# Optimization experiments

Measured on AMD Instinct MI355X. Metric: run time of the kernel, lower is better.

The kernel has to match this reference:

```python
import jax, jax.numpy as jnp
import numpy as np

N_FEAT = 256
NUM_HEADS = 8
EPS = 1e-12  # torch F.normalize default eps


def setup_inputs() -> dict:
    key = jax.random.key(0)
    k1, k2, k3 = jax.random.split(key, 3)
    b, c, h, w = 1, N_FEAT, 64, 64
    x = jax.random.normal(k1, (b, c, h, w), dtype=jnp.float32)
    # 1x1 convs == channel GEMMs; store as (out_ch, in_ch) matrices
    w_qkv = jax.random.normal(k2, (3 * c, c), dtype=jnp.float32) * (1.0 / np.sqrt(c))
    w_proj = jax.random.normal(k3, (c, c), dtype=jnp.float32) * (1.0 / np.sqrt(c))
    temperature = jnp.ones((NUM_HEADS, 1, 1), dtype=jnp.float32)
    return {"x": x, "w_qkv": w_qkv, "w_proj": w_proj, "temperature": temperature}


def _l2norm(t):
    n = jnp.linalg.norm(t, axis=-1, keepdims=True)
    return t / jnp.maximum(n, EPS)


def reference(x, w_qkv, w_proj, temperature):
    b, c, h, w = x.shape
    heads = temperature.shape[0]
    d = c // heads
    hw = h * w
    xf = x.reshape(b, c, hw)
    # qkv 1x1 conv: (b, 3c, hw)
    qkv = jnp.einsum('oc,bcs->bos', w_qkv, xf)
    qkv = qkv.reshape(b, 3, heads, d, hw)
    q, k, v = qkv[:, 0], qkv[:, 1], qkv[:, 2]  # (b, heads, d, hw)
    q = jnp.swapaxes(q, -2, -1)  # (b, heads, hw, d)
    k = jnp.swapaxes(k, -2, -1)
    v = jnp.swapaxes(v, -2, -1)
    q = _l2norm(q)
    k = _l2norm(k)
    attn = jnp.einsum('bhsd,bhtd->bhst', q, k) * temperature[None]  # (b, heads, hw, hw)
    attn = jax.nn.softmax(attn, axis=-1)
    out = jnp.einsum('bhst,bhtd->bhsd', attn, v)  # (b, heads, hw, d)
    # faithful to torch: permute(0,2,1,3).reshape(b,c,h,w)
    out = out.transpose(0, 2, 1, 3).reshape(b, c, h, w)
    out = jnp.einsum('oc,bchw->bohw', w_proj, out)
    return out
```

## Files before the change

kernel.cpp:

```cpp
#include <hip/hip_runtime.h>
#include <stdint.h>

#define HW 4096
#define NH 8
#define NSPLIT 4
#define TSPLIT (HW / NSPLIT)

typedef __attribute__((ext_vector_type(8))) short short8;
typedef __attribute__((ext_vector_type(4))) short s4b;
typedef __attribute__((ext_vector_type(4))) float floatx4;

__device__ inline float bf2f(uint16_t u) {
  union { uint32_t i; float f; } v; v.i = ((uint32_t)u) << 16; return v.f;
}
__device__ inline uint16_t f2bf(float f) {
  union { float f; uint32_t i; } v; v.f = f;
  uint32_t u = v.i; u += 0x7fffu + ((u >> 16) & 1u); return (uint16_t)(u >> 16);
}
__device__ inline uint32_t pk2(float a, float b) {
  return (uint32_t)f2bf(a) | ((uint32_t)f2bf(b) << 16);
}
__device__ inline uint32_t asu(float f) { union { float f; uint32_t i; } v; v.f = f; return v.i; }
__device__ inline uint32_t pk2r(float a, float b) {
#if __has_builtin(__builtin_amdgcn_cvt_pk_bf16_f32)
  union { short2 s; uint32_t u; } x;
  x.s = __builtin_amdgcn_cvt_pk_bf16_f32(a, b);
  return x.u;
#else
  return __builtin_amdgcn_perm(asu(b) + 0x8000u, asu(a) + 0x8000u, 0x07060302u);
#endif
}
__device__ inline s4b mk_s4(uint32_t lo, uint32_t hi) {
  union { uint32_t u[2]; s4b s; } x; x.u[0] = lo; x.u[1] = hi; return x.s;
}
__device__ inline floatx4 mfma16(s4b a, s4b b, floatx4 c) {
#if __has_builtin(__builtin_amdgcn_mfma_f32_16x16x16bf16_1k)
  return __builtin_amdgcn_mfma_f32_16x16x16bf16_1k(a, b, c, 0, 0, 0);
#else
  floatx4 d = c;
  asm volatile("v_mfma_f32_16x16x16_bf16 %0, %1, %2, %0" : "+v"(d) : "v"(a), "v"(b));
  return d;
#endif
}
__device__ inline bool is_f32(const uint32_t* Tp32) { return (Tp32[0] & 0xFFFFu) == 0u; }
__device__ inline float read_temp(const void* Tp, int h) {
  if (is_f32((const uint32_t*)Tp)) return ((const float*)Tp)[h];
  return bf2f(((const uint16_t*)Tp)[h]);
}

__global__ __launch_bounds__(256) void k_transpose(const void* __restrict__ X,
                                                   uint16_t* __restrict__ Xt,
                                                   const uint32_t* __restrict__ Tp32) {
  __shared__ uint16_t tile[64 * 66];
  int t = threadIdx.x;
  int s0 = blockIdx.x * 64, c0 = blockIdx.y * 64;
  {
    int cl = t >> 2, sc = (t & 3) * 16;
    uint32_t* l32 = (uint32_t*)tile;
    int base = (cl * 66 + sc) >> 1;
    if (is_f32(Tp32)) {
      const float4* x4 = (const float4*)((const float*)X + (c0 + cl) * HW + s0 + sc);
      float4 a = x4[0], b = x4[1], c = x4[2], d = x4[3];
      l32[base + 0] = pk2(a.x, a.y); l32[base + 1] = pk2(a.z, a.w);
      l32[base + 2] = pk2(b.x, b.y); l32[base + 3] = pk2(b.z, b.w);
      l32[base + 4] = pk2(c.x, c.y); l32[base + 5] = pk2(c.z, c.w);
      l32[base + 6] = pk2(d.x, d.y); l32[base + 7] = pk2(d.z, d.w);
    } else {
      const uint4* xp = (const uint4*)((const uint16_t*)X + (c0 + cl) * HW + s0 + sc);
      uint4 a = xp[0], b = xp[1];
      l32[base + 0] = a.x; l32[base + 1] = a.y; l32[base + 2] = a.z; l32[base + 3] = a.w;
      l32[base + 4] = b.x; l32[base + 5] = b.y; l32[base + 6] = b.z; l32[base + 7] = b.w;
    }
  }
  __syncthreads();
  {
    int sl = t >> 2, cc = (t & 3) * 16;
    uint32_t wbuf[8];
#pragma unroll
    for (int j = 0; j < 8; ++j) {
      uint32_t lo = tile[(cc + 2 * j) * 66 + sl];
      uint32_t hi = tile[(cc + 2 * j + 1) * 66 + sl];
      wbuf[j] = lo | (hi << 16);
    }
    uint4* op = (uint4*)(Xt + (s0 + sl) * 256 + c0 + cc);
    op[0] = make_uint4(wbuf[0], wbuf[1], wbuf[2], wbuf[3]);
    op[1] = make_uint4(wbuf[4], wbuf[5], wbuf[6], wbuf[7]);
  }
}

__global__ __launch_bounds__(256) void k_gemm_qkv(const void* __restrict__ A,
                                                  const uint16_t* __restrict__ Bt,
                                                  const void* __restrict__ Tp,
                                                  uint16_t* __restrict__ Qr,
                                                  uint16_t* __restrict__ Kr,
                                                  uint16_t* __restrict__ Vr) {
  __shared__ uint16_t sA[128 * 64];
  __shared__ uint16_t sB[64 * 64];
  int tid = threadIdx.x;
  int w = tid >> 6, lane = tid & 63, lm = lane & 15, qd = lane >> 4;
  int n0 = blockIdx.x * 64, m0 = blockIdx.y * 128;
  bool aF32 = is_f32((const uint32_t*)Tp);
  floatx4 acc[2][4];
#pragma unroll
  for (int i = 0; i < 2; ++i)
#pragma unroll
    for (int j = 0; j < 4; ++j) acc[i][j] = (floatx4){0.f, 0.f, 0.f, 0.f};

  for (int k0 = 0; k0 < 256; k0 += 64) {
    __syncthreads();
#pragma unroll
    for (int r = 0; r < 4; ++r) {
      int ch = r * 256 + tid; int row = ch >> 3, c8 = ch & 7;
      uint4 v;
      if (aF32) {
        const float4* s4 = (const float4*)((const float*)A + (m0 + row) * 256 + k0 + c8 * 8);
        float4 a = s4[0], b = s4[1];
        v = make_uint4(pk2(a.x, a.y), pk2(a.z, a.w), pk2(b.x, b.y), pk2(b.z, b.w));
      } else {
        v = *(const uint4*)((const uint16_t*)A + (m0 + row) * 256 + k0 + c8 * 8);
      }
      *(uint4*)(&sA[row * 64 + (c8 ^ (row & 7)) * 8]) = v;
    }
#pragma unroll
    for (int r = 0; r < 2; ++r) {
      int ch = r * 256 + tid; int row = ch >> 3, c8 = ch & 7;
      uint4 v = *(const uint4*)(Bt + (n0 + row) * 256 + k0 + c8 * 8);
      *(uint4*)(&sB[row * 64 + (c8 ^ (row & 7)) * 8]) = v;
    }
    __syncthreads();
#pragma unroll
    for (int kk = 0; kk < 2; ++kk) {
      short8 af[2];
#pragma unroll
      for (int mt = 0; mt < 2; ++mt) {
        int row = w * 32 + mt * 16 + lm;
        af[mt] = *(const short8*)(&sA[row * 64 + ((kk * 4 + qd) ^ (row & 7)) * 8]);
      }
#pragma unroll
      for (int nt = 0; nt < 4; ++nt) {
        int row = nt * 16 + lm;
        short8 bf = *(const short8*)(&sB[row * 64 + ((kk * 4 + qd) ^ (row & 7)) * 8]);
#pragma unroll
        for (int mt = 0; mt < 2; ++mt)
          acc[mt][nt] = __builtin_amdgcn_mfma_f32_16x16x32_bf16(af[mt], bf, acc[mt][nt], 0, 0, 0);
      }
    }
  }
  int ow = m0 + w * 32;
  int type = ow >> 8;
  int hh = (ow >> 5) & 7;
  float tv = read_temp(Tp, hh);
#pragma unroll
  for (int nt = 0; nt < 4; ++nt) {
    int s = n0 + nt * 16 + lm;
    if (type < 2) {
      float ssq = 0.f;
#pragma unroll
      for (int mt = 0; mt < 2; ++mt)
#pragma unroll
        for (int r = 0; r < 4; ++r) ssq += acc[mt][nt][r] * acc[mt][nt][r];
      ssq += __shfl_xor(ssq, 16, 64);
      ssq += __shfl_xor(ssq, 32, 64);
      float sc = (type == 0 ? tv : 1.0f) / fmaxf(sqrtf(ssq), 1e-12f);
      uint16_t* dst = (type == 0 ? Qr : Kr) + ((hh << 12) + s) * 32;
#pragma unroll
      for (int mt = 0; mt < 2; ++mt)
        *(uint2*)(dst + mt * 16 + qd * 4) =
            make_uint2(pk2r(acc[mt][nt][0] * sc, acc[mt][nt][1] * sc),
                       pk2r(acc[mt][nt][2] * sc, acc[mt][nt][3] * sc));
    } else {
#pragma unroll
      for (int mt = 0; mt < 2; ++mt)
#pragma unroll
        for (int r = 0; r < 4; ++r)
          Vr[(hh * 32 + mt * 16 + qd * 4 + r) * HW + s] = f2bf(acc[mt][nt][r]);
    }
  }
}

__global__ __launch_bounds__(256, 8) void k_attn(const uint16_t* __restrict__ Qr,
                                                 const uint16_t* __restrict__ Kr,
                                                 const uint16_t* __restrict__ Vr,
                                                 const void* __restrict__ Tp,
                                                 float* __restrict__ Op,
                                                 float* __restrict__ Lp) {
  __shared__ uint16_t sK[128 * 32];
  __shared__ uint16_t sV[32 * 128];
  int tid = threadIdx.x;
  int w = tid >> 6, lane = tid & 63, lm = lane & 15, qd = lane >> 4;
  int bid = blockIdx.x;
  int h = bid & 7;
  int j = bid >> 3;
  int sp = j & 3;
  int qb = j >> 2;
  int srow = qb * 64 + w * 16;
  const float c1 = 1.44269504088896340736f;
  float c2 = fabsf(read_temp(Tp, h)) * c1;
  short8 qf = *(const short8*)(Qr + ((h << 12) + srow + lm) * 32 + qd * 8);
  const uint16_t* Kg = Kr + (h << 12) * 32;
  const uint16_t* Vg = Vr + (h * 32) * HW;
  floatx4 o0 = {0.f, 0.f, 0.f, 0.f}, o1 = {0.f, 0.f, 0.f, 0.f};
  floatx4 l0 = {0.f, 0.f, 0.f, 0.f};
  const s4b ones = mk_s4(0x3F803F80u, 0x3F803F80u);

  int rK = tid >> 2, cK = tid & 3;
  uint16_t* dK0 = &sK[rK * 32 + (cK ^ ((rK >> 1) & 3)) * 8];
  uint16_t* dK1 = &sK[(rK + 64) * 32 + (cK ^ (((rK + 64) >> 1) & 3)) * 8];
  const uint16_t* gK0 = Kg + (sp * TSPLIT + rK) * 32 + cK * 8;
  const uint16_t* gK1 = gK0 + 64 * 32;
  int dV = tid >> 4, cV = tid & 15;
  bool sw = dV & 1;
  uint16_t* dV0 = &sV[dV * 128 + (cV ^ ((dV >> 1) & 7)) * 8];
  uint16_t* dV1 = &sV[(dV + 16) * 128 + (cV ^ (((dV + 16) >> 1) & 7)) * 8];
  const uint16_t* gV0 = Vg + dV * HW + sp * TSPLIT + cV * 8;
  const uint16_t* gV1 = gV0 + 16 * HW;

  uint4 rk0 = *(const uint4*)gK0, rk1 = *(const uint4*)gK1;
  uint4 rv0 = *(const uint4*)gV0, rv1 = *(const uint4*)gV1;

  for (int i = 0; i < TSPLIT / 128; ++i) {
    __syncthreads();
    *(uint4*)dK0 = rk0;
    *(uint4*)dK1 = rk1;
    *(uint4*)dV0 = sw ? make_uint4(rv0.z, rv0.w, rv0.x, rv0.y) : rv0;
    *(uint4*)dV1 = sw ? make_uint4(rv1.z, rv1.w, rv1.x, rv1.y) : rv1;
    if (i + 1 < TSPLIT / 128) {
      gK0 += 128 * 32; gK1 += 128 * 32; gV0 += 128; gV1 += 128;
      rk0 = *(const uint4*)gK0; rk1 = *(const uint4*)gK1;
      rv0 = *(const uint4*)gV0; rv1 = *(const uint4*)gV1;
    }
    asm volatile("s_waitcnt lgkmcnt(0)\n\ts_barrier" ::: "memory");
#pragma unroll
    for (int nt = 0; nt < 8; ++nt) {
      int krow = nt * 16 + lm;
      short8 kf = *(const short8*)(&sK[krow * 32 + (qd ^ ((lm >> 1) & 3)) * 8]);
      int gp = (nt * 4 + qd) ^ lm;
      s4b v0 = *(const s4b*)(&sV[lm * 128 + gp * 4]);
      s4b v1 = *(const s4b*)(&sV[(lm + 16) * 128 + gp * 4]);
      floatx4 z = {0.f, 0.f, 0.f, 0.f};
      floatx4 sv = __builtin_amdgcn_mfma_f32_16x16x32_bf16(kf, qf, z, 0, 0, 0);
      float p0 = __builtin_amdgcn_exp2f(fmaf(sv[0], c1, -c2));
      float p1 = __builtin_amdgcn_exp2f(fmaf(sv[1], c1, -c2));
      float p2 = __builtin_amdgcn_exp2f(fmaf(sv[2], c1, -c2));
      float p3 = __builtin_amdgcn_exp2f(fmaf(sv[3], c1, -c2));
      s4b pa = mk_s4(pk2r(p0, p1), pk2r(p2, p3));
      o0 = mfma16(pa, v0, o0);
      o1 = mfma16(pa, v1, o1);
      l0 = mfma16(pa, ones, l0);
    }
  }
  int sb = (sp * NH + h) * HW + srow;
  float* op = Op + (size_t)sb * 32;
#pragma unroll
  for (int r = 0; r < 4; ++r) {
    op[(qd * 4 + r) * 32 + lm] = o0[r];
    op[(qd * 4 + r) * 32 + 16 + lm] = o1[r];
  }
  if (lm == 0) {
#pragma unroll
    for (int r = 0; r < 4; ++r) Lp[sb + qd * 4 + r] = l0[r];
  }
}

__global__ __launch_bounds__(256) void k_comb(const float* __restrict__ Op,
                                              const float* __restrict__ Lp,
                                              uint16_t* __restrict__ Yt) {
  int gid = blockIdx.x * 256 + threadIdx.x;
  int g = gid >> 2, d0 = (gid & 3) * 8;
  int h = g >> 12, s = g & 4095;
  float L = 0.f;
  float a[8];
#pragma unroll
  for (int j = 0; j < 8; ++j) a[j] = 0.f;
#pragma unroll
  for (int sp = 0; sp < NSPLIT; ++sp) {
    int gj = sp * NH * HW + g;
    L += Lp[gj];
    const float4* p = (const float4*)(Op + (size_t)gj * 32 + d0);
    float4 x = p[0], y = p[1];
    a[0] += x.x; a[1] += x.y; a[2] += x.z; a[3] += x.w;
    a[4] += y.x; a[5] += y.y; a[6] += y.z; a[7] += y.w;
  }
  float inv = __builtin_amdgcn_rcpf(L);
  int pbase = ((s & 15) << 8) + h * 32 + d0;
  int cp = s >> 4;
#pragma unroll
  for (int j = 0; j < 8; ++j) Yt[(pbase + j) * 256 + cp] = f2bf(a[j] * inv);
}

__global__ __launch_bounds__(256) void k_gemm_proj(const void* __restrict__ A,
                                                   const uint16_t* __restrict__ Bt,
                                                   void* __restrict__ C,
                                                   const uint32_t* __restrict__ Tp32) {
  __shared__ uint16_t sA[64 * 64];
  __shared__ uint16_t sB[64 * 64];
  int tid = threadIdx.x;
  int w = tid >> 6, lane = tid & 63, lm = lane & 15, qd = lane >> 4;
  int n0 = blockIdx.x * 64, m0 = blockIdx.y * 64;
  bool aF32 = is_f32(Tp32);
  floatx4 acc[4];
#pragma unroll
  for (int i = 0; i < 4; ++i) acc[i] = (floatx4){0.f, 0.f, 0.f, 0.f};

  for (int k0 = 0; k0 < 256; k0 += 64) {
    __syncthreads();
#pragma unroll
    for (int r = 0; r < 2; ++r) {
      int ch = r * 256 + tid; int row = ch >> 3, c8 = ch & 7;
      uint4 v;
      if (aF32) {
        const float4* s4 = (const float4*)((const float*)A + (m0 + row) * 256 + k0 + c8 * 8);
        float4 a = s4[0], b = s4[1];
        v = make_uint4(pk2(a.x, a.y), pk2(a.z, a.w), pk2(b.x, b.y), pk2(b.z, b.w));
      } else {
        v = *(const uint4*)((const uint16_t*)A + (m0 + row) * 256 + k0 + c8 * 8);
      }
      *(uint4*)(&sA[row * 64 + (c8 ^ (row & 7)) * 8]) = v;
    }
#pragma unroll
    for (int r = 0; r < 2; ++r) {
      int ch = r * 256 + tid; int row = ch >> 3, c8 = ch & 7;
      uint4 v = *(const uint4*)(Bt + (n0 + row) * 256 + k0 + c8 * 8);
      *(uint4*)(&sB[row * 64 + (c8 ^ (row & 7)) * 8]) = v;
    }
    __syncthreads();
#pragma unroll
    for (int kk = 0; kk < 2; ++kk) {
      int arow = w * 16 + lm;
      short8 af = *(const short8*)(&sA[arow * 64 + ((kk * 4 + qd) ^ (arow & 7)) * 8]);
#pragma unroll
      for (int nt = 0; nt < 4; ++nt) {
        int row = nt * 16 + lm;
        short8 bf = *(const short8*)(&sB[row * 64 + ((kk * 4 + qd) ^ (row & 7)) * 8]);
        acc[nt] = __builtin_amdgcn_mfma_f32_16x16x32_bf16(af, bf, acc[nt], 0, 0, 0);
      }
    }
  }
  bool f32o = is_f32(Tp32);
#pragma unroll
  for (int nt = 0; nt < 4; ++nt)
#pragma unroll
    for (int r = 0; r < 4; ++r) {
      int row = m0 + w * 16 + qd * 4 + r;
      int col = n0 + nt * 16 + lm;
      if (f32o) ((float*)C)[row * HW + col] = acc[nt][r];
      else ((uint16_t*)C)[row * HW + col] = f2bf(acc[nt][r]);
    }
}

extern "C" void kernel_launch(void* const* d_in, const int* in_sizes, int n_in,
                              void* d_out, int out_size, void* d_ws, size_t ws_size,
                              hipStream_t stream) {
  const void* X  = d_in[0];
  const void* Wq = d_in[1];
  const void* Wp = d_in[2];
  const void* Tp = d_in[3];
  const uint32_t* Tp32 = (const uint32_t*)Tp;
  uint16_t* ws = (uint16_t*)d_ws;
  uint16_t* Xt = ws;
  uint16_t* Qr = Xt + 4096 * 256;
  uint16_t* Kr = Qr + NH * HW * 32;
  uint16_t* Vr = Kr + NH * HW * 32;
  uint16_t* Yt = Vr + NH * 32 * HW;
  float* Op = (float*)(Yt + 4096 * 256);
  float* Lp = Op + (size_t)NSPLIT * NH * HW * 32;

  k_transpose<<<dim3(64, 4), 256, 0, stream>>>(X, Xt, Tp32);
  k_gemm_qkv<<<dim3(64, 6), 256, 0, stream>>>(Wq, Xt, Tp, Qr, Kr, Vr);
  k_attn<<<dim3(2048), 256, 0, stream>>>(Qr, Kr, Vr, Tp, Op, Lp);
  k_comb<<<dim3(512), 256, 0, stream>>>(Op, Lp, Yt);
  k_gemm_proj<<<dim3(64, 4), 256, 0, stream>>>(Wp, Yt, d_out, Tp32);
}
```

Baseline: 130.3 us.

## Process two query tiles per wave in attention and store partials as bf16

Each attention wave now handles 32 query rows instead of 16. Every K/V tile loaded into shared memory is reused for two Q fragments, which halves the grid and the K/V traffic per query. Partial outputs are written as bf16 instead of fp32, which halves the partial-result traffic between the attention and combine kernels. The combine kernel is widened to 16 channels per thread to match. The costs are more registers per wave (launch bound lowered to 4 blocks) and some precision lost in the partial sums.

New measurement: 122.2 us. -6.2%, faster.

```diff
diff --git a/kernel.cpp b/kernel.cpp
--- a/kernel.cpp
+++ b/kernel.cpp
@@ -12,6 +12,12 @@
 
 __device__ inline float bf2f(uint16_t u) {
   union { uint32_t i; float f; } v; v.i = ((uint32_t)u) << 16; return v.f;
+}
+__device__ inline float bflo(uint32_t u) {
+  union { uint32_t i; float f; } v; v.i = u << 16; return v.f;
+}
+__device__ inline float bfhi(uint32_t u) {
+  union { uint32_t i; float f; } v; v.i = u & 0xFFFF0000u; return v.f;
 }
 __device__ inline uint16_t f2bf(float f) {
   union { float f; uint32_t i; } v; v.f = f;
@@ -178,11 +184,11 @@
   }
 }
 
-__global__ __launch_bounds__(256, 8) void k_attn(const uint16_t* __restrict__ Qr,
+__global__ __launch_bounds__(256, 4) void k_attn(const uint16_t* __restrict__ Qr,
                                                  const uint16_t* __restrict__ Kr,
                                                  const uint16_t* __restrict__ Vr,
                                                  const void* __restrict__ Tp,
-                                                 float* __restrict__ Op,
+                                                 uint16_t* __restrict__ Op,
                                                  float* __restrict__ Lp) {
   __shared__ uint16_t sK[128 * 32];
   __shared__ uint16_t sV[32 * 128];
@@ -193,14 +199,16 @@
   int j = bid >> 3;
   int sp = j & 3;
   int qb = j >> 2;
-  int srow = qb * 64 + w * 16;
+  int srow = qb * 128 + w * 32;
   const float c1 = 1.44269504088896340736f;
   float c2 = fabsf(read_temp(Tp, h)) * c1;
-  short8 qf = *(const short8*)(Qr + ((h << 12) + srow + lm) * 32 + qd * 8);
+  short8 qf0 = *(const short8*)(Qr + ((h << 12) + srow + lm) * 32 + qd * 8);
+  short8 qf1 = *(const short8*)(Qr + ((h << 12) + srow + 16 + lm) * 32 + qd * 8);
   const uint16_t* Kg = Kr + (h << 12) * 32;
   const uint16_t* Vg = Vr + (h * 32) * HW;
-  floatx4 o0 = {0.f, 0.f, 0.f, 0.f}, o1 = {0.f, 0.f, 0.f, 0.f};
-  floatx4 l0 = {0.f, 0.f, 0.f, 0.f};
+  floatx4 o00 = {0.f, 0.f, 0.f, 0.f}, o01 = {0.f, 0.f, 0.f, 0.f};
+  floatx4 o10 = {0.f, 0.f, 0.f, 0.f}, o11 = {0.f, 0.f, 0.f, 0.f};
+  floatx4 l0 = {0.f, 0.f, 0.f, 0.f}, l1 = {0.f, 0.f, 0.f, 0.f};
   const s4b ones = mk_s4(0x3F803F80u, 0x3F803F80u);
 
   int rK = tid >> 2, cK = tid & 3;
@@ -238,54 +246,70 @@
       s4b v0 = *(const s4b*)(&sV[lm * 128 + gp * 4]);
       s4b v1 = *(const s4b*)(&sV[(lm + 16) * 128 + gp * 4]);
       floatx4 z = {0.f, 0.f, 0.f, 0.f};
-      floatx4 sv = __builtin_amdgcn_mfma_f32_16x16x32_bf16(kf, qf, z, 0, 0, 0);
+      floatx4 sv = __builtin_amdgcn_mfma_f32_16x16x32_bf16(kf, qf0, z, 0, 0, 0);
       float p0 = __builtin_amdgcn_exp2f(fmaf(sv[0], c1, -c2));
       float p1 = __builtin_amdgcn_exp2f(fmaf(sv[1], c1, -c2));
       float p2 = __builtin_amdgcn_exp2f(fmaf(sv[2], c1, -c2));
       float p3 = __builtin_amdgcn_exp2f(fmaf(sv[3], c1, -c2));
       s4b pa = mk_s4(pk2r(p0, p1), pk2r(p2, p3));
-      o0 = mfma16(pa, v0, o0);
-      o1 = mfma16(pa, v1, o1);
+      o00 = mfma16(pa, v0, o00);
+      o01 = mfma16(pa, v1, o01);
       l0 = mfma16(pa, ones, l0);
+      sv = __builtin_amdgcn_mfma_f32_16x16x32_bf16(kf, qf1, z, 0, 0, 0);
+      p0 = __builtin_amdgcn_exp2f(fmaf(sv[0], c1, -c2));
+      p1 = __builtin_amdgcn_exp2f(fmaf(sv[1], c1, -c2));
+      p2 = __builtin_amdgcn_exp2f(fmaf(sv[2], c1, -c2));
+      p3 = __builtin_amdgcn_exp2f(fmaf(sv[3], c1, -c2));
+      pa = mk_s4(pk2r(p0, p1), pk2r(p2, p3));
+      o10 = mfma16(pa, v0, o10);
+      o11 = mfma16(pa, v1, o11);
+      l1 = mfma16(pa, ones, l1);
     }
   }
   int sb = (sp * NH + h) * HW + srow;
-  float* op = Op + (size_t)sb * 32;
+  uint16_t* op = Op + (size_t)sb * 32;
 #pragma unroll
   for (int r = 0; r < 4; ++r) {
-    op[(qd * 4 + r) * 32 + lm] = o0[r];
-    op[(qd * 4 + r) * 32 + 16 + lm] = o1[r];
+    op[(qd * 4 + r) * 32 + lm] = f2bf(o00[r]);
+    op[(qd * 4 + r) * 32 + 16 + lm] = f2bf(o01[r]);
+    op[(16 + qd * 4 + r) * 32 + lm] = f2bf(o10[r]);
+    op[(16 + qd * 4 + r) * 32 + 16 + lm] = f2bf(o11[r]);
   }
   if (lm == 0) {
 #pragma unroll
-    for (int r = 0; r < 4; ++r) Lp[sb + qd * 4 + r] = l0[r];
-  }
-}
-
-__global__ __launch_bounds__(256) void k_comb(const float* __restrict__ Op,
+    for (int r = 0; r < 4; ++r) {
+      Lp[sb + qd * 4 + r] = l0[r];
+      Lp[sb + 16 + qd * 4 + r] = l1[r];
+    }
+  }
+}
+
+__global__ __launch_bounds__(256) void k_comb(const uint16_t* __restrict__ Op,
                                               const float* __restrict__ Lp,
                                               uint16_t* __restrict__ Yt) {
   int gid = blockIdx.x * 256 + threadIdx.x;
-  int g = gid >> 2, d0 = (gid & 3) * 8;
+  int g = gid >> 1, d0 = (gid & 1) * 16;
   int h = g >> 12, s = g & 4095;
   float L = 0.f;
-  float a[8];
-#pragma unroll
-  for (int j = 0; j < 8; ++j) a[j] = 0.f;
+  float a[16];
+#pragma unroll
+  for (int j = 0; j < 16; ++j) a[j] = 0.f;
 #pragma unroll
   for (int sp = 0; sp < NSPLIT; ++sp) {
     int gj = sp * NH * HW + g;
     L += Lp[gj];
-    const float4* p = (const float4*)(Op + (size_t)gj * 32 + d0);
-    float4 x = p[0], y = p[1];
-    a[0] += x.x; a[1] += x.y; a[2] += x.z; a[3] += x.w;
-    a[4] += y.x; a[5] += y.y; a[6] += y.z; a[7] += y.w;
+    const uint4* p = (const uint4*)(Op + (size_t)gj * 32 + d0);
+    uint4 x = p[0], y = p[1];
+    a[0] += bflo(x.x); a[1] += bfhi(x.x); a[2] += bflo(x.y); a[3] += bfhi(x.y);
+    a[4] += bflo(x.z); a[5] += bfhi(x.z); a[6] += bflo(x.w); a[7] += bfhi(x.w);
+    a[8] += bflo(y.x); a[9] += bfhi(y.x); a[10] += bflo(y.y); a[11] += bfhi(y.y);
+    a[12] += bflo(y.z); a[13] += bfhi(y.z); a[14] += bflo(y.w); a[15] += bfhi(y.w);
   }
   float inv = __builtin_amdgcn_rcpf(L);
   int pbase = ((s & 15) << 8) + h * 32 + d0;
   int cp = s >> 4;
 #pragma unroll
-  for (int j = 0; j < 8; ++j) Yt[(pbase + j) * 256 + cp] = f2bf(a[j] * inv);
+  for (int j = 0; j < 16; ++j) Yt[(pbase + j) * 256 + cp] = f2bf(a[j] * inv);
 }
 
 __global__ __launch_bounds__(256) void k_gemm_proj(const void* __restrict__ A,
@@ -362,12 +386,12 @@
   uint16_t* Kr = Qr + NH * HW * 32;
   uint16_t* Vr = Kr + NH * HW * 32;
   uint16_t* Yt = Vr + NH * 32 * HW;
-  float* Op = (float*)(Yt + 4096 * 256);
-  float* Lp = Op + (size_t)NSPLIT * NH * HW * 32;
+  uint16_t* Op = Yt + 4096 * 256;
+  float* Lp = (float*)(Op + (size_t)NSPLIT * NH * HW * 32);
 
   k_transpose<<<dim3(64, 4), 256, 0, stream>>>(X, Xt, Tp32);
   k_gemm_qkv<<<dim3(64, 6), 256, 0, stream>>>(Wq, Xt, Tp, Qr, Kr, Vr);
-  k_attn<<<dim3(2048), 256, 0, stream>>>(Qr, Kr, Vr, Tp, Op, Lp);
-  k_comb<<<dim3(512), 256, 0, stream>>>(Op, Lp, Yt);
+  k_attn<<<dim3(1024), 256, 0, stream>>>(Qr, Kr, Vr, Tp, Op, Lp);
+  k_comb<<<dim3(256), 256, 0, stream>>>(Op, Lp, Yt);
   k_gemm_proj<<<dim3(64, 4), 256, 0, stream>>>(Wp, Yt, d_out, Tp32);
 }
```
